# Kernel tuning notes

Hardware: AMD Instinct MI355X
Metric: run time of the kernel (lower is better)

The kernel has to match this reference:

```python
import jax, jax.numpy as jnp
import numpy as np

N_NODES = 100000
N_EDGES = 1600000
EMBED_DIM = 64
NUM_HEADS = 4
HEAD_DIM = EMBED_DIM // NUM_HEADS  # 16


def mish(x):
    return x * jnp.tanh(jax.nn.softplus(x))


def setup_inputs() -> dict:
    key = jax.random.key(0)
    ks = jax.random.split(key, 8)
    x = jax.random.normal(ks[0], (N_NODES, EMBED_DIM), dtype=jnp.float32)
    senders = jax.random.randint(ks[1], (N_EDGES,), 0, N_NODES, dtype=jnp.int32)
    receivers = jax.random.randint(ks[2], (N_EDGES,), 0, N_NODES, dtype=jnp.int32)
    sc = 1.0 / np.sqrt(EMBED_DIM)
    # DenseGeneral(features=(H, d)) for senders / receivers, with bias
    Ws = jax.random.normal(ks[3], (EMBED_DIM, NUM_HEADS, HEAD_DIM), dtype=jnp.float32) * sc
    bs = jnp.zeros((NUM_HEADS, HEAD_DIM), dtype=jnp.float32)
    Wr = jax.random.normal(ks[4], (EMBED_DIM, NUM_HEADS, HEAD_DIM), dtype=jnp.float32) * sc
    br = jnp.zeros((NUM_HEADS, HEAD_DIM), dtype=jnp.float32)
    # Dense(1) on last axis (head_dim), weights shared across heads
    aw = jax.random.normal(ks[5], (HEAD_DIM,), dtype=jnp.float32) * (1.0 / np.sqrt(HEAD_DIM))
    ab = jnp.zeros((1,), dtype=jnp.float32)
    return {"x": x, "Ws": Ws, "bs": bs, "Wr": Wr, "br": br,
            "aw": aw, "ab": ab, "senders": senders, "receivers": receivers}


def reference(x, Ws, bs, Wr, br, aw, ab, senders, receivers):
    n = x.shape[0]
    # Node-level projections (same math as per-edge DenseGeneral, less traffic)
    s_proj = jnp.einsum('nf,fhd->nhd', x, Ws) + bs  # [N,H,d]
    r_proj = jnp.einsum('nf,fhd->nhd', x, Wr) + br  # [N,H,d]
    se = s_proj[senders]      # [E,H,d] gather of sender features
    re = r_proj[receivers]    # [E,H,d] gather of receiver features
    # GATv2 logit: Dense(1)(mish(s + r)) -> [E,H]
    logits = jnp.einsum('ehd,d->eh', mish(se + re), aw) + ab[0]
    # Segment softmax over incoming edges of each receiver node
    lmax = jax.ops.segment_max(logits, receivers, num_segments=n)
    ex = jnp.exp(logits - lmax[receivers])
    denom = jax.ops.segment_sum(ex, receivers, num_segments=n)
    alpha = ex / denom[receivers]  # [E,H]
    # Scatter-sum weighted sender features back to receiver nodes
    out = jax.ops.segment_sum(alpha[..., None] * se, receivers, num_segments=n)  # [N,H,d]
    return out.reshape(n, -1)  # [N, H*d]
```

## Files before the change

### kernel.cpp

```cpp
#include <hip/hip_runtime.h>
#include <hip/hip_fp16.h>
#include <math.h>

#define N_NODES 100000
#define N_EDGES 1600000
#define EMBED 64
#define HEADS 4
#define HDIM 16

#define SLOTS 64

#define BKT_SHIFT 8
#define BKT_NODES 256
#define NBKT 391
#define BKT_CAP 5120
#define TILE 4096
#define NTILE 391
#define NGRP (N_EDGES / 4)

#define LOG2E 1.44269504f

__device__ __forceinline__ float mish_aw(float z, float awc) {
    float ex  = __expf(fminf(z, 30.f));
    float u   = 1.f + ex;
    float den = fmaf(u, u, 1.f);
    float f   = fmaf(-2.f, __builtin_amdgcn_rcpf(den), 1.f);
    return z * awc * f;
}

template<int CTRL>
__device__ __forceinline__ float ror_add(float t) {
    int x = __builtin_amdgcn_mov_dpp(__float_as_int(t), CTRL, 0xF, 0xF, true);
    return t + __int_as_float(x);
}
__device__ __forceinline__ float head_reduce(float t) {
    t = ror_add<0x121>(t);
    t = ror_add<0x122>(t);
    t = ror_add<0x124>(t);
    t = ror_add<0x128>(t);
    return t;
}

template<int CTRL>
__device__ __forceinline__ __half2 hror_add(__half2 t) {
    int x = __builtin_amdgcn_mov_dpp(__builtin_bit_cast(int, t), CTRL, 0xF, 0xF, true);
    return __hadd2(t, __builtin_bit_cast(__half2, x));
}
__device__ __forceinline__ __half2 head_reduce_h2(__half2 t) {
    t = hror_add<0x121>(t);
    t = hror_add<0x122>(t);
    t = hror_add<0x124>(t);
    t = hror_add<0x128>(t);
    return t;
}

__global__ __launch_bounds__(256) void proj_kernel(
        const float* __restrict__ x,
        const float* __restrict__ Ws, const float* __restrict__ bs,
        const float* __restrict__ Wr, const float* __restrict__ br,
        unsigned short* __restrict__ sph, unsigned short* __restrict__ rph) {
    __shared__ float wsT[64 * 68];
    __shared__ float wrT[64 * 68];
    __shared__ float xsh[16 * 68];
    int tid = threadIdx.x;
    for (int i = tid; i < 4096; i += 256) {
        int k = i >> 6, o = i & 63;
        wsT[o * 68 + k] = Ws[i];
        wrT[o * 68 + k] = Wr[i];
    }
    int nb = blockIdx.x << 4;
    {
        float4 v = ((const float4*)(x + ((size_t)nb << 6)))[tid];
        int n  = tid >> 4;
        int k4 = tid & 15;
        *(float4*)(xsh + n * 68 + (k4 << 2)) = v;
    }
    __syncthreads();
    int o = tid & 63;
    int w = tid >> 6;
    float bsv = bs[o], brv = br[o];
    float accs[4], accr[4];
#pragma unroll
    for (int p = 0; p < 4; ++p) { accs[p] = bsv; accr[p] = brv; }
    const float4* ws4 = (const float4*)wsT + o * 17;
    const float4* wr4 = (const float4*)wrT + o * 17;
    const float4* xs4 = (const float4*)xsh + (w << 2) * 17;
#pragma unroll
    for (int k4 = 0; k4 < 16; ++k4) {
        float4 a = ws4[k4];
        float4 b = wr4[k4];
#pragma unroll
        for (int p = 0; p < 4; ++p) {
            float4 xv = xs4[p * 17 + k4];
            accs[p] += xv.x * a.x + xv.y * a.y + xv.z * a.z + xv.w * a.w;
            accr[p] += xv.x * b.x + xv.y * b.y + xv.z * b.z + xv.w * b.w;
        }
    }
#pragma unroll
    for (int p = 0; p < 4; ++p) {
        int node = nb + (w << 2) + p;
        sph[(node << 6) + o] = __half_as_ushort(__float2half_rn(accs[p]));
        rph[(node << 6) + o] = __half_as_ushort(__float2half_rn(accr[p]));
    }
}

__global__ __launch_bounds__(256) void bucketa_kernel(
        const int* __restrict__ senders, const int* __restrict__ receivers,
        int* __restrict__ bktcnt, int* __restrict__ bkt) {
    __shared__ int hist[NBKT];
    __shared__ int base[NBKT];
    __shared__ int cur[NBKT];
    int tid = threadIdx.x;
    for (int i = tid; i < NBKT; i += 256) hist[i] = 0;
    __syncthreads();
    int g0 = blockIdx.x * (TILE / 4);
    int4 r[4], s[4];
    bool v[4];
#pragma unroll
    for (int t = 0; t < 4; ++t) {
        int g = g0 + t * 256 + tid;
        v[t] = (g < NGRP);
        if (v[t]) {
            r[t] = ((const int4*)receivers)[g];
            s[t] = ((const int4*)senders)[g];
            atomicAdd(&hist[r[t].x >> BKT_SHIFT], 1);
            atomicAdd(&hist[r[t].y >> BKT_SHIFT], 1);
            atomicAdd(&hist[r[t].z >> BKT_SHIFT], 1);
            atomicAdd(&hist[r[t].w >> BKT_SHIFT], 1);
        }
    }
    __syncthreads();
    for (int i = tid; i < NBKT; i += 256) {
        int h = hist[i];
        base[i] = (h > 0) ? atomicAdd(&bktcnt[i], h) : 0;
        cur[i] = 0;
    }
    __syncthreads();
#pragma unroll
    for (int t = 0; t < 4; ++t) {
        if (v[t]) {
            int b, rk, slot;
            b = r[t].x >> BKT_SHIFT; rk = atomicAdd(&cur[b], 1); slot = base[b] + rk;
            if (slot < BKT_CAP) bkt[b * BKT_CAP + slot] = ((r[t].x & (BKT_NODES - 1)) << 17) | s[t].x;
            b = r[t].y >> BKT_SHIFT; rk = atomicAdd(&cur[b], 1); slot = base[b] + rk;
            if (slot < BKT_CAP) bkt[b * BKT_CAP + slot] = ((r[t].y & (BKT_NODES - 1)) << 17) | s[t].y;
            b = r[t].z >> BKT_SHIFT; rk = atomicAdd(&cur[b], 1); slot = base[b] + rk;
            if (slot < BKT_CAP) bkt[b * BKT_CAP + slot] = ((r[t].z & (BKT_NODES - 1)) << 17) | s[t].z;
            b = r[t].w >> BKT_SHIFT; rk = atomicAdd(&cur[b], 1); slot = base[b] + rk;
            if (slot < BKT_CAP) bkt[b * BKT_CAP + slot] = ((r[t].w & (BKT_NODES - 1)) << 17) | s[t].w;
        }
    }
}

__global__ __launch_bounds__(1024) void bucketb_kernel(
        const int* __restrict__ bktcnt, const int* __restrict__ bkt,
        int* __restrict__ cursor, int* __restrict__ csr) {
    __shared__ int lcur[BKT_NODES];
    int tid = threadIdx.x;
    int b = blockIdx.x;
    if (tid < BKT_NODES) lcur[tid] = 0;
    __syncthreads();
    int cnt = bktcnt[b];
    if (cnt > BKT_CAP) cnt = BKT_CAP;
    const int* bb = bkt + b * BKT_CAP;
    for (int i = tid; i < cnt; i += 1024) {
        int vv = bb[i];
        int rl = vv >> 17;
        int sv = vv & 0x1FFFF;
        int slot = atomicAdd(&lcur[rl], 1);
        if (slot < SLOTS) csr[((((b << BKT_SHIFT) + rl)) << 6) + slot] = sv << 7;
    }
    __syncthreads();
    if (tid < BKT_NODES) {
        int node = (b << BKT_SHIFT) + tid;
        if (node < N_NODES) cursor[node] = lcur[tid];
    }
}

__global__ __launch_bounds__(256) void fused_gather_kernel(
                                    const unsigned short* __restrict__ sph,
                                    const unsigned short* __restrict__ rph,
                                    const int* __restrict__ csr,
                                    const int* __restrict__ cursor,
                                    const float* __restrict__ aw,
                                    const float* __restrict__ ab,
                                    float* __restrict__ out) {
    int wave = (blockIdx.x * blockDim.x + threadIdx.x) >> 6;
    int lane = threadIdx.x & 63;
    int deg = cursor[wave];
    deg = (deg > SLOTS) ? SLOTS : deg;
    int myoff = csr[(wave << 6) + lane];
    const char* splb = (const char*)sph + (lane << 1);
    float rp  = __half2float(__ushort_as_half(rph[(wave << 6) + lane]));
    float awc = aw[lane & 15];
    float abl = ab[0] * LOG2E;
    __half2 k_pk    = __float2half2_rn(0.5f * LOG2E);
    __half2 rpk_pk  = __float2half2_rn(rp * 0.5f * LOG2E);
    __half2 aw_pk   = __float2half2_rn(awc);
    __half2 rpa_pk  = __float2half2_rn(rp * awc);
    __half2 ones    = __float2half2_rn(1.0f);
    __half2 neg2    = __float2half2_rn(-2.0f);
    float l = 0.f, acc = 0.f;
    int i = 0;
    for (; i + 8 <= deg; i += 8) {
        int o_[8];
        unsigned short su[8];
#pragma unroll
        for (int j = 0; j < 8; ++j) o_[j] = __builtin_amdgcn_readlane(myoff, i + j);
#pragma unroll
        for (int j = 0; j < 8; ++j) su[j] = *(const unsigned short*)(splb + o_[j]);
#pragma unroll
        for (int j = 0; j < 4; ++j) {
            __half2 sp  = __halves2half2(__ushort_as_half(su[2 * j]),
                                         __ushort_as_half(su[2 * j + 1]));
            __half2 arg = __hfma2(sp, k_pk, rpk_pk);
            __half2 t2  = h2exp2(arg);
            __half2 w   = __hmul2(t2, t2);
            __half2 u   = __hadd2(w, ones);
            __half2 den = __hfma2(u, u, ones);
            __half2 r   = h2rcp(den);
            __half2 f   = __hfma2(neg2, r, ones);
            __half2 za  = __hfma2(sp, aw_pk, rpa_pk);
            __half2 tt  = head_reduce_h2(__hmul2(za, f));
            float p0 = __builtin_amdgcn_exp2f(fmaf(__low2float(tt),  LOG2E, abl));
            float p1 = __builtin_amdgcn_exp2f(fmaf(__high2float(tt), LOG2E, abl));
            l += p0 + p1;
            acc = fmaf(p0, __low2float(sp), fmaf(p1, __high2float(sp), acc));
        }
    }
    for (; i + 2 <= deg; i += 2) {
        int o0 = __builtin_amdgcn_readlane(myoff, i);
        int o1 = __builtin_amdgcn_readlane(myoff, i + 1);
        __half2 sp  = __halves2half2(__ushort_as_half(*(const unsigned short*)(splb + o0)),
                                     __ushort_as_half(*(const unsigned short*)(splb + o1)));
        __half2 arg = __hfma2(sp, k_pk, rpk_pk);
        __half2 t2  = h2exp2(arg);
        __half2 w   = __hmul2(t2, t2);
        __half2 u   = __hadd2(w, ones);
        __half2 den = __hfma2(u, u, ones);
        __half2 r   = h2rcp(den);
        __half2 f   = __hfma2(neg2, r, ones);
        __half2 za  = __hfma2(sp, aw_pk, rpa_pk);
        __half2 tt  = head_reduce_h2(__hmul2(za, f));
        float p0 = __builtin_amdgcn_exp2f(fmaf(__low2float(tt),  LOG2E, abl));
        float p1 = __builtin_amdgcn_exp2f(fmaf(__high2float(tt), LOG2E, abl));
        l += p0 + p1;
        acc = fmaf(p0, __low2float(sp), fmaf(p1, __high2float(sp), acc));
    }
    if (i < deg) {
        int o0 = __builtin_amdgcn_readlane(myoff, i);
        float sp0 = __half2float(__ushort_as_half(*(const unsigned short*)(splb + o0)));
        float t0 = head_reduce(mish_aw(sp0 + rp, awc));
        float p = __builtin_amdgcn_exp2f(fmaf(t0, LOG2E, abl));
        l += p;
        acc = fmaf(p, sp0, acc);
    }
    out[(wave << 6) + lane] = (deg > 0) ? acc * __builtin_amdgcn_rcpf(l) : 0.f;
}

extern "C" void kernel_launch(void* const* d_in, const int* in_sizes, int n_in,
                              void* d_out, int out_size, void* d_ws, size_t ws_size,
                              hipStream_t stream) {
    const float* x  = (const float*)d_in[0];
    const float* Ws = (const float*)d_in[1];
    const float* bs = (const float*)d_in[2];
    const float* Wr = (const float*)d_in[3];
    const float* br = (const float*)d_in[4];
    const float* aw = (const float*)d_in[5];
    const float* ab = (const float*)d_in[6];
    const int* senders   = (const int*)d_in[7];
    const int* receivers = (const int*)d_in[8];
    float* out = (float*)d_out;

    char* wsp = (char*)d_ws;
    unsigned short* sph = (unsigned short*)wsp;  wsp += (size_t)N_NODES * EMBED * 2;
    unsigned short* rph = (unsigned short*)wsp;  wsp += (size_t)N_NODES * EMBED * 2;
    int* csr    = (int*)wsp;  wsp += (size_t)N_NODES * SLOTS * 4;
    int* cursor = (int*)wsp;  wsp += (size_t)N_NODES * 4;
    int* bkt    = (int*)wsp;  wsp += (size_t)NBKT * BKT_CAP * 4;
    int* bktcnt = (int*)wsp;  wsp += 512 * 4;

    hipMemsetAsync(bktcnt, 0, NBKT * 4, stream);

    proj_kernel<<<N_NODES / 16, 256, 0, stream>>>(x, Ws, bs, Wr, br, sph, rph);

    bucketa_kernel<<<NTILE, 256, 0, stream>>>(senders, receivers, bktcnt, bkt);
    bucketb_kernel<<<NBKT, 1024, 0, stream>>>(bktcnt, bkt, cursor, csr);

    int gather_blocks = (N_NODES * 64 + 255) / 256;
    fused_gather_kernel<<<gather_blocks, 256, 0, stream>>>(sph, rph, csr, cursor,
                                                           aw, ab, out);
}
```

Measured before the change: 145.1 us.

## Merge projection and bucketing kernels; load CSR offsets as scalar loads

Merges the node projection kernel and the first edge-bucketing pass into one launch, with block index selecting the role, so the two independent stages can run concurrently and one launch is removed. In the gather kernel the wave index is made uniform via readfirstlane, and per-edge sender offsets are read directly from the CSR row, likely as scalar loads, instead of a per-lane vector load plus readlane. The fused kernel sizes shared memory for the larger projection role, which may limit occupancy for the bucketing blocks, and scalar loads add scalar memory latency inside the edge loop.

```diff
diff --git a/kernel.cpp b/kernel.cpp
--- a/kernel.cpp
+++ b/kernel.cpp
@@ -18,6 +18,9 @@
 #define NTILE 391
 #define NGRP (N_EDGES / 4)
 
+#define NBLK_PROJ (N_NODES / 16)
+#define SMEM_BYTES 39168
+
 #define LOG2E 1.44269504f
 
 __device__ __forceinline__ float mish_aw(float z, float awc) {
@@ -54,100 +57,100 @@
     return t;
 }
 
-__global__ __launch_bounds__(256) void proj_kernel(
+__global__ __launch_bounds__(256) void proj_bucketa_kernel(
         const float* __restrict__ x,
         const float* __restrict__ Ws, const float* __restrict__ bs,
         const float* __restrict__ Wr, const float* __restrict__ br,
-        unsigned short* __restrict__ sph, unsigned short* __restrict__ rph) {
-    __shared__ float wsT[64 * 68];
-    __shared__ float wrT[64 * 68];
-    __shared__ float xsh[16 * 68];
+        const int* __restrict__ senders, const int* __restrict__ receivers,
+        unsigned short* __restrict__ sph, unsigned short* __restrict__ rph,
+        int* __restrict__ bktcnt, int* __restrict__ bkt) {
+    __shared__ __align__(16) char smem[SMEM_BYTES];
     int tid = threadIdx.x;
-    for (int i = tid; i < 4096; i += 256) {
-        int k = i >> 6, o = i & 63;
-        wsT[o * 68 + k] = Ws[i];
-        wrT[o * 68 + k] = Wr[i];
-    }
-    int nb = blockIdx.x << 4;
-    {
-        float4 v = ((const float4*)(x + ((size_t)nb << 6)))[tid];
-        int n  = tid >> 4;
-        int k4 = tid & 15;
-        *(float4*)(xsh + n * 68 + (k4 << 2)) = v;
-    }
-    __syncthreads();
-    int o = tid & 63;
-    int w = tid >> 6;
-    float bsv = bs[o], brv = br[o];
-    float accs[4], accr[4];
-#pragma unroll
-    for (int p = 0; p < 4; ++p) { accs[p] = bsv; accr[p] = brv; }
-    const float4* ws4 = (const float4*)wsT + o * 17;
-    const float4* wr4 = (const float4*)wrT + o * 17;
-    const float4* xs4 = (const float4*)xsh + (w << 2) * 17;
-#pragma unroll
-    for (int k4 = 0; k4 < 16; ++k4) {
-        float4 a = ws4[k4];
-        float4 b = wr4[k4];
+    if (blockIdx.x < NBLK_PROJ) {
+        float* wsT = (float*)smem;
+        float* wrT = wsT + 64 * 68;
+        float* xsh = wrT + 64 * 68;
+        for (int i = tid; i < 4096; i += 256) {
+            int k = i >> 6, o = i & 63;
+            wsT[o * 68 + k] = Ws[i];
+            wrT[o * 68 + k] = Wr[i];
+        }
+        int nb = blockIdx.x << 4;
+        {
+            float4 v = ((const float4*)(x + ((size_t)nb << 6)))[tid];
+            int n  = tid >> 4;
+            int k4 = tid & 15;
+            *(float4*)(xsh + n * 68 + (k4 << 2)) = v;
+        }
+        __syncthreads();
+        int o = tid & 63;
+        int w = tid >> 6;
+        float bsv = bs[o], brv = br[o];
+        float accs[4], accr[4];
+#pragma unroll
+        for (int p = 0; p < 4; ++p) { accs[p] = bsv; accr[p] = brv; }
+        const float4* ws4 = (const float4*)wsT + o * 17;
+        const float4* wr4 = (const float4*)wrT + o * 17;
+        const float4* xs4 = (const float4*)xsh + (w << 2) * 17;
+#pragma unroll
+        for (int k4 = 0; k4 < 16; ++k4) {
+            float4 a = ws4[k4];
+            float4 b = wr4[k4];
+#pragma unroll
+            for (int p = 0; p < 4; ++p) {
+                float4 xv = xs4[p * 17 + k4];
+                accs[p] += xv.x * a.x + xv.y * a.y + xv.z * a.z + xv.w * a.w;
+                accr[p] += xv.x * b.x + xv.y * b.y + xv.z * b.z + xv.w * b.w;
+            }
+        }
 #pragma unroll
         for (int p = 0; p < 4; ++p) {
-            float4 xv = xs4[p * 17 + k4];
-            accs[p] += xv.x * a.x + xv.y * a.y + xv.z * a.z + xv.w * a.w;
-            accr[p] += xv.x * b.x + xv.y * b.y + xv.z * b.z + xv.w * b.w;
-        }
-    }
-#pragma unroll
-    for (int p = 0; p < 4; ++p) {
-        int node = nb + (w << 2) + p;
-        sph[(node << 6) + o] = __half_as_ushort(__float2half_rn(accs[p]));
-        rph[(node << 6) + o] = __half_as_ushort(__float2half_rn(accr[p]));
-    }
-}
-
-__global__ __launch_bounds__(256) void bucketa_kernel(
-        const int* __restrict__ senders, const int* __restrict__ receivers,
-        int* __restrict__ bktcnt, int* __restrict__ bkt) {
-    __shared__ int hist[NBKT];
-    __shared__ int base[NBKT];
-    __shared__ int cur[NBKT];
-    int tid = threadIdx.x;
-    for (int i = tid; i < NBKT; i += 256) hist[i] = 0;
-    __syncthreads();
-    int g0 = blockIdx.x * (TILE / 4);
-    int4 r[4], s[4];
-    bool v[4];
-#pragma unroll
-    for (int t = 0; t < 4; ++t) {
-        int g = g0 + t * 256 + tid;
-        v[t] = (g < NGRP);
-        if (v[t]) {
-            r[t] = ((const int4*)receivers)[g];
-            s[t] = ((const int4*)senders)[g];
-            atomicAdd(&hist[r[t].x >> BKT_SHIFT], 1);
-            atomicAdd(&hist[r[t].y >> BKT_SHIFT], 1);
-            atomicAdd(&hist[r[t].z >> BKT_SHIFT], 1);
-            atomicAdd(&hist[r[t].w >> BKT_SHIFT], 1);
-        }
-    }
-    __syncthreads();
-    for (int i = tid; i < NBKT; i += 256) {
-        int h = hist[i];
-        base[i] = (h > 0) ? atomicAdd(&bktcnt[i], h) : 0;
-        cur[i] = 0;
-    }
-    __syncthreads();
-#pragma unroll
-    for (int t = 0; t < 4; ++t) {
-        if (v[t]) {
-            int b, rk, slot;
-            b = r[t].x >> BKT_SHIFT; rk = atomicAdd(&cur[b], 1); slot = base[b] + rk;
-            if (slot < BKT_CAP) bkt[b * BKT_CAP + slot] = ((r[t].x & (BKT_NODES - 1)) << 17) | s[t].x;
-            b = r[t].y >> BKT_SHIFT; rk = atomicAdd(&cur[b], 1); slot = base[b] + rk;
-            if (slot < BKT_CAP) bkt[b * BKT_CAP + slot] = ((r[t].y & (BKT_NODES - 1)) << 17) | s[t].y;
-            b = r[t].z >> BKT_SHIFT; rk = atomicAdd(&cur[b], 1); slot = base[b] + rk;
-            if (slot < BKT_CAP) bkt[b * BKT_CAP + slot] = ((r[t].z & (BKT_NODES - 1)) << 17) | s[t].z;
-            b = r[t].w >> BKT_SHIFT; rk = atomicAdd(&cur[b], 1); slot = base[b] + rk;
-            if (slot < BKT_CAP) bkt[b * BKT_CAP + slot] = ((r[t].w & (BKT_NODES - 1)) << 17) | s[t].w;
+            int node = nb + (w << 2) + p;
+            sph[(node << 6) + o] = __half_as_ushort(__float2half_rn(accs[p]));
+            rph[(node << 6) + o] = __half_as_ushort(__float2half_rn(accr[p]));
+        }
+    } else {
+        int* hist = (int*)smem;
+        int* base = hist + NBKT;
+        int* cur  = base + NBKT;
+        for (int i = tid; i < NBKT; i += 256) hist[i] = 0;
+        __syncthreads();
+        int g0 = (blockIdx.x - NBLK_PROJ) * (TILE / 4);
+        int4 r[4], s[4];
+        bool v[4];
+#pragma unroll
+        for (int t = 0; t < 4; ++t) {
+            int g = g0 + t * 256 + tid;
+            v[t] = (g < NGRP);
+            if (v[t]) {
+                r[t] = ((const int4*)receivers)[g];
+                s[t] = ((const int4*)senders)[g];
+                atomicAdd(&hist[r[t].x >> BKT_SHIFT], 1);
+                atomicAdd(&hist[r[t].y >> BKT_SHIFT], 1);
+                atomicAdd(&hist[r[t].z >> BKT_SHIFT], 1);
+                atomicAdd(&hist[r[t].w >> BKT_SHIFT], 1);
+            }
+        }
+        __syncthreads();
+        for (int i = tid; i < NBKT; i += 256) {
+            int h = hist[i];
+            base[i] = (h > 0) ? atomicAdd(&bktcnt[i], h) : 0;
+            cur[i] = 0;
+        }
+        __syncthreads();
+#pragma unroll
+        for (int t = 0; t < 4; ++t) {
+            if (v[t]) {
+                int b, rk, slot;
+                b = r[t].x >> BKT_SHIFT; rk = atomicAdd(&cur[b], 1); slot = base[b] + rk;
+                if (slot < BKT_CAP) bkt[b * BKT_CAP + slot] = ((r[t].x & (BKT_NODES - 1)) << 17) | s[t].x;
+                b = r[t].y >> BKT_SHIFT; rk = atomicAdd(&cur[b], 1); slot = base[b] + rk;
+                if (slot < BKT_CAP) bkt[b * BKT_CAP + slot] = ((r[t].y & (BKT_NODES - 1)) << 17) | s[t].y;
+                b = r[t].z >> BKT_SHIFT; rk = atomicAdd(&cur[b], 1); slot = base[b] + rk;
+                if (slot < BKT_CAP) bkt[b * BKT_CAP + slot] = ((r[t].z & (BKT_NODES - 1)) << 17) | s[t].z;
+                b = r[t].w >> BKT_SHIFT; rk = atomicAdd(&cur[b], 1); slot = base[b] + rk;
+                if (slot < BKT_CAP) bkt[b * BKT_CAP + slot] = ((r[t].w & (BKT_NODES - 1)) << 17) | s[t].w;
+            }
         }
     }
 }
@@ -186,10 +189,11 @@
                                     const float* __restrict__ ab,
                                     float* __restrict__ out) {
     int wave = (blockIdx.x * blockDim.x + threadIdx.x) >> 6;
+    wave = __builtin_amdgcn_readfirstlane(wave);
     int lane = threadIdx.x & 63;
     int deg = cursor[wave];
     deg = (deg > SLOTS) ? SLOTS : deg;
-    int myoff = csr[(wave << 6) + lane];
+    const int* cbase = csr + (wave << 6);
     const char* splb = (const char*)sph + (lane << 1);
     float rp  = __half2float(__ushort_as_half(rph[(wave << 6) + lane]));
     float awc = aw[lane & 15];
@@ -203,12 +207,9 @@
     float l = 0.f, acc = 0.f;
     int i = 0;
     for (; i + 8 <= deg; i += 8) {
-        int o_[8];
         unsigned short su[8];
 #pragma unroll
-        for (int j = 0; j < 8; ++j) o_[j] = __builtin_amdgcn_readlane(myoff, i + j);
-#pragma unroll
-        for (int j = 0; j < 8; ++j) su[j] = *(const unsigned short*)(splb + o_[j]);
+        for (int j = 0; j < 8; ++j) su[j] = *(const unsigned short*)(splb + cbase[i + j]);
 #pragma unroll
         for (int j = 0; j < 4; ++j) {
             __half2 sp  = __halves2half2(__ushort_as_half(su[2 * j]),
@@ -229,10 +230,8 @@
         }
     }
     for (; i + 2 <= deg; i += 2) {
-        int o0 = __builtin_amdgcn_readlane(myoff, i);
-        int o1 = __builtin_amdgcn_readlane(myoff, i + 1);
-        __half2 sp  = __halves2half2(__ushort_as_half(*(const unsigned short*)(splb + o0)),
-                                     __ushort_as_half(*(const unsigned short*)(splb + o1)));
+        __half2 sp  = __halves2half2(__ushort_as_half(*(const unsigned short*)(splb + cbase[i])),
+                                     __ushort_as_half(*(const unsigned short*)(splb + cbase[i + 1])));
         __half2 arg = __hfma2(sp, k_pk, rpk_pk);
         __half2 t2  = h2exp2(arg);
         __half2 w   = __hmul2(t2, t2);
@@ -248,8 +247,7 @@
         acc = fmaf(p0, __low2float(sp), fmaf(p1, __high2float(sp), acc));
     }
     if (i < deg) {
-        int o0 = __builtin_amdgcn_readlane(myoff, i);
-        float sp0 = __half2float(__ushort_as_half(*(const unsigned short*)(splb + o0)));
+        float sp0 = __half2float(__ushort_as_half(*(const unsigned short*)(splb + cbase[i])));
         float t0 = head_reduce(mish_aw(sp0 + rp, awc));
         float p = __builtin_amdgcn_exp2f(fmaf(t0, LOG2E, abl));
         l += p;
@@ -282,9 +280,9 @@
 
     hipMemsetAsync(bktcnt, 0, NBKT * 4, stream);
 
-    proj_kernel<<<N_NODES / 16, 256, 0, stream>>>(x, Ws, bs, Wr, br, sph, rph);
-
-    bucketa_kernel<<<NTILE, 256, 0, stream>>>(senders, receivers, bktcnt, bkt);
+    proj_bucketa_kernel<<<NBLK_PROJ + NTILE, 256, 0, stream>>>(
+        x, Ws, bs, Wr, br, senders, receivers, sph, rph, bktcnt, bkt);
+
     bucketb_kernel<<<NBKT, 1024, 0, stream>>>(bktcnt, bkt, cursor, csr);
 
     int gather_blocks = (N_NODES * 64 + 255) / 256;
```

Measured after the change: 133.5 us. 8.0% less time.
